# Kernel optimization log

Measured on AMD Instinct MI355X. Metric: run time of the kernel, lower is better.

Reference implementation:

```python
import jax, jax.numpy as jnp
import numpy as np

B, C, K, D = 8192, 64, 256, 64  # batch, ncodebooks, ncentroids, subvect_len
BN_EPS = 1e-5


def setup_inputs() -> dict:
    key = jax.random.key(0)
    k1, k2 = jax.random.split(key)
    return {
        "inputs": jax.random.normal(k1, (B, C, D), dtype=jnp.float32),
        "centroids_k": jax.random.normal(k2, (C, K, D), dtype=jnp.float32) * 0.1,
        "bn_gamma": jnp.ones((C,), dtype=jnp.float32),
        "bn_beta": jnp.zeros((C,), dtype=jnp.float32),
    }


def _response(inputs, centroids_k, bn_gamma, bn_beta):
    # dot-metric scores: (B, C, K)
    r = jnp.einsum('bcd,ckd->bck', inputs, centroids_k)
    # BatchNorm1d over channel dim C (training mode: biased batch stats over B and K)
    mean = r.mean(axis=(0, 2), keepdims=True)
    var = ((r - mean) ** 2).mean(axis=(0, 2), keepdims=True)
    r = (r - mean) * jax.lax.rsqrt(var + BN_EPS)
    return r * bn_gamma[None, :, None] + bn_beta[None, :, None]


def reference(inputs, centroids_k, bn_gamma, bn_beta):
    r = _response(inputs, centroids_k, bn_gamma, bn_beta)
    # torch.max(response, -1) -> (values, indices)
    mse = r.max(axis=-1)                 # (B, C)
    codes = jnp.argmax(r, axis=-1)       # (B, C) int
    # tie_in_n_out=True: _centroids_v is _centroids_k
    return codes, mse, centroids_k
```

## Files before the change

kernel.cpp:

```cpp
#include <hip/hip_runtime.h>

#define B_  8192
#define C_  64
#define K_  256
#define D_  64
#define NBT 2
#define GX  (B_ / (256 * NBT))
#define BC_ (B_ * C_)
#define BN_EPS 1e-5

#define WCAP_C 1024
#define DELTA  2.5e-3f

typedef _Float16 f16x8 __attribute__((ext_vector_type(8)));
typedef float    f32x4 __attribute__((ext_vector_type(4)));

__device__ __forceinline__ int swz(int row, int dbyte) {
    return (row * 128 + dbyte) ^ ((row & 7) << 4);
}

__global__ __launch_bounds__(512, 6) void dpq_mfma(
    const float* __restrict__ x,
    const float* __restrict__ cent,
    const float* __restrict__ gamma,
    float* __restrict__ out,
    float* __restrict__ part_sum,
    float* __restrict__ part_sq,
    int* __restrict__ wcount,
    int* __restrict__ worklist)
{
    __shared__ char lds[32768];
    const int c   = blockIdx.y;
    const int tid = threadIdx.x;
    const float sgn = (gamma[c] < 0.0f) ? -1.0f : 1.0f;

    {
        const int row = tid >> 1, half = tid & 1;
        const float* g = cent + ((size_t)c * K_ + row) * D_ + half * 32;
#pragma unroll
        for (int q = 0; q < 4; ++q) {
            float4 u0 = *(const float4*)(g + q * 8);
            float4 u1 = *(const float4*)(g + q * 8 + 4);
            f16x8 h;
            h[0] = (_Float16)(u0.x * sgn); h[1] = (_Float16)(u0.y * sgn);
            h[2] = (_Float16)(u0.z * sgn); h[3] = (_Float16)(u0.w * sgn);
            h[4] = (_Float16)(u1.x * sgn); h[5] = (_Float16)(u1.y * sgn);
            h[6] = (_Float16)(u1.z * sgn); h[7] = (_Float16)(u1.w * sgn);
            *(f16x8*)(lds + swz(row, half * 64 + q * 16)) = h;
        }
    }

    const int wid = tid >> 6, lane = tid & 63;
    const int col = lane & 15, grp = lane >> 4;

    float accs = 0.0f, accq = 0.0f;
    bool first = true;

    for (int bt = 0; bt < NBT; ++bt) {
        const int b0 = (blockIdx.x * NBT + bt) * 256 + wid * 32;

        f16x8 xf[2][2];
#pragma unroll
        for (int T = 0; T < 2; ++T)
#pragma unroll
            for (int S = 0; S < 2; ++S) {
                const float* xr = x + ((size_t)(b0 + T * 16 + col) * C_ + c) * D_
                                    + S * 32 + grp * 8;
                float4 u0 = *(const float4*)xr;
                float4 u1 = *(const float4*)(xr + 4);
                f16x8 h;
                h[0] = (_Float16)u0.x; h[1] = (_Float16)u0.y;
                h[2] = (_Float16)u0.z; h[3] = (_Float16)u0.w;
                h[4] = (_Float16)u1.x; h[5] = (_Float16)u1.y;
                h[6] = (_Float16)u1.z; h[7] = (_Float16)u1.w;
                xf[T][S] = h;
            }
        if (first) { __syncthreads(); first = false; }

        float best[2] = {-3.4e38f, -3.4e38f};
        float sec [2] = {-3.4e38f, -3.4e38f};
        int   bk_ [2] = {0, 0};

#pragma unroll 4
        for (int t = 0; t < 16; ++t) {
            const f16x8 a0 = *(const f16x8*)(lds + swz(t * 16 + col,      grp * 16));
            const f16x8 a1 = *(const f16x8*)(lds + swz(t * 16 + col, 64 + grp * 16));
            const int kb = t * 16 + grp * 4;
#pragma unroll
            for (int T = 0; T < 2; ++T) {
                f32x4 acc = {0.f, 0.f, 0.f, 0.f};
                acc = __builtin_amdgcn_mfma_f32_16x16x32_f16(a0, xf[T][0], acc, 0, 0, 0);
                acc = __builtin_amdgcn_mfma_f32_16x16x32_f16(a1, xf[T][1], acc, 0, 0, 0);
#pragma unroll
                for (int j = 0; j < 4; ++j) {
                    const float r = acc[j];
                    accs += r;
                    accq = fmaf(r, r, accq);
                    const bool gt = r > best[T];
                    sec[T]  = __builtin_amdgcn_fmed3f(r, best[T], sec[T]);
                    best[T] = fmaxf(best[T], r);
                    bk_[T]  = gt ? kb + j : bk_[T];
                }
            }
        }

#pragma unroll
        for (int T = 0; T < 2; ++T) {
            float bv = best[T], sv = sec[T];
            int   bk = bk_[T];
#pragma unroll
            for (int m = 16; m <= 32; m <<= 1) {
                const float ov = __shfl_xor(bv, m);
                const int   ok = __shfl_xor(bk, m);
                const float os = __shfl_xor(sv, m);
                sv = fmaxf(fmaxf(sv, os), fminf(bv, ov));
                if (ov > bv || (ov == bv && ok < bk)) bk = ok;
                bv = fmaxf(bv, ov);
            }
            if (grp == 0) {
                const int b = b0 + T * 16 + col;
                const size_t idx = (size_t)b * C_ + c;
                out[idx] = (float)bk;
                out[(size_t)BC_ + idx] = bv;
                if (bv - sv < DELTA && worklist) {
                    const int slot = atomicAdd(&wcount[c], 1);
                    if (slot < WCAP_C) worklist[c * WCAP_C + slot] = b;
                }
            }
        }
    }

#pragma unroll
    for (int m = 1; m <= 32; m <<= 1) {
        accs += __shfl_xor(accs, m);
        accq += __shfl_xor(accq, m);
    }
    __syncthreads();
    float* red = (float*)lds;
    if (lane == 0) { red[wid] = accs; red[8 + wid] = accq; }
    __syncthreads();
    if (tid == 0) {
        float s = 0.f, q = 0.f;
#pragma unroll
        for (int w = 0; w < 8; ++w) { s += red[w]; q += red[8 + w]; }
        part_sum[c * GX + blockIdx.x] = s;
        part_sq [c * GX + blockIdx.x] = q;
    }
}

__global__ __launch_bounds__(256) void dpq_referee(
    const float* __restrict__ x,
    const float* __restrict__ cent,
    const float* __restrict__ gamma,
    const int* __restrict__ wcount,
    const int* __restrict__ worklist,
    float* __restrict__ out)
{
    __shared__ float cl[K_ * D_];
    const int c = blockIdx.x;
    int n = wcount[c];
    if (n > WCAP_C) n = WCAP_C;
    if (n == 0) return;
    const int t = threadIdx.x;
    const float sgnf = (gamma[c] < 0.0f) ? -1.0f : 1.0f;

    {
        const float* g = cent + ((size_t)c * K_ + t) * D_;
#pragma unroll 8
        for (int d = 0; d < D_; ++d)
            cl[t * D_ + (d ^ (t & 31))] = g[d];
    }
    __syncthreads();

    const int wid = t >> 6, lane = t & 63;
    for (int i = blockIdx.y * 4 + wid; i < n; i += gridDim.y * 4) {
        const int b = worklist[c * WCAP_C + i];
        const float* xr = x + ((size_t)b * C_ + c) * D_;
        double bv = -1.0e300;
        int bk = 0;
#pragma unroll
        for (int q = 0; q < 4; ++q) {
            const int k = q * 64 + lane;
            const int sw = k & 31;
            double s = 0.0;
#pragma unroll 8
            for (int d = 0; d < D_; ++d)
                s += (double)xr[d] * (double)cl[k * D_ + (d ^ sw)];
            s *= (double)sgnf;
            if (s > bv) { bv = s; bk = k; }
        }
#pragma unroll
        for (int m = 1; m <= 32; m <<= 1) {
            const double ov = __shfl_xor(bv, m);
            const int   ok = __shfl_xor(bk, m);
            if (ov > bv || (ov == bv && ok < bk)) { bv = ov; bk = ok; }
        }
        if (lane == 0) {
            const size_t idx = (size_t)b * C_ + c;
            out[idx] = (float)bk;
            out[(size_t)BC_ + idx] = (float)bv;
        }
    }
}

__global__ void dpq_stats(
    const float* __restrict__ part_sum,
    const float* __restrict__ part_sq,
    const float* __restrict__ gamma,
    const float* __restrict__ beta,
    float* __restrict__ scale_out,
    float* __restrict__ shift_out)
{
    const int c = threadIdx.x;
    if (c >= C_) return;
    double s = 0.0, q = 0.0;
    for (int i = 0; i < GX; ++i) {
        s += (double)part_sum[c * GX + i];
        q += (double)part_sq [c * GX + i];
    }
    const double n    = (double)B_ * (double)K_;
    const double mean = s / n;
    const double var  = q / n - mean * mean;
    const double sc   = fabs((double)gamma[c]) / sqrt(var + BN_EPS);
    scale_out[c] = (float)sc;
    shift_out[c] = (float)((double)beta[c] - mean * sc);
}

__global__ __launch_bounds__(256) void dpq_apply(
    float* __restrict__ out,
    const float* __restrict__ scale,
    const float* __restrict__ shift)
{
    const int idx = blockIdx.x * 256 + threadIdx.x;
    const int c = idx & (C_ - 1);
    const float sc = scale[c];
    const float sh = shift[c];
    if (sc == 0.0f) {
        out[idx] = 0.0f;
        out[(size_t)BC_ + idx] = sh;
    } else {
        out[(size_t)BC_ + idx] = fmaf(out[(size_t)BC_ + idx], sc, sh);
    }
}

extern "C" void kernel_launch(void* const* d_in, const int* in_sizes, int n_in,
                              void* d_out, int out_size, void* d_ws, size_t ws_size,
                              hipStream_t stream)
{
    const float* x     = (const float*)d_in[0];
    const float* cent  = (const float*)d_in[1];
    const float* gamma = (const float*)d_in[2];
    const float* beta  = (const float*)d_in[3];
    float* out = (float*)d_out;
    float* ws  = (float*)d_ws;

    float* part_sum = ws;
    float* part_sq  = ws + 1024;
    float* scale    = ws + 2048;
    float* shift    = ws + 2112;
    int*   wcount   = (int*)(ws + 2176);
    int*   worklist = (int*)(ws + 2240);
    const size_t need = (size_t)(2240 + C_ * WCAP_C) * 4;
    if (ws_size < need) { wcount = nullptr; worklist = nullptr; }

    if (wcount)
        hipMemsetAsync(wcount, 0, C_ * sizeof(int), stream);

    dim3 g1(GX, C_);
    hipLaunchKernelGGL(dpq_mfma, g1, dim3(512), 0, stream,
                       x, cent, gamma, out, part_sum, part_sq, wcount, worklist);
    if (wcount)
        hipLaunchKernelGGL(dpq_referee, dim3(C_, 8), dim3(256), 0, stream,
                           x, cent, gamma, wcount, worklist, out);
    hipLaunchKernelGGL(dpq_stats, dim3(1), dim3(64), 0, stream,
                       part_sum, part_sq, gamma, beta, scale, shift);
    hipLaunchKernelGGL(dpq_apply, dim3(BC_ / 256), dim3(256), 0, stream,
                       out, scale, shift);
    hipMemcpyAsync(out + 2 * (size_t)BC_, cent,
                   (size_t)C_ * K_ * D_ * sizeof(float),
                   hipMemcpyDeviceToDevice, stream);
}
```

Before: 101.0 us.

## Process four row tiles per warp and pack argmax index into float low bits

Each warp now handles 64 batch rows (four 16-row tiles) per step instead of 32, so every LDS centroid fragment feeds twice as many MFMAs. The argmax index is packed into the low 8 mantissa bits of the score, which lets best/second tracking run as pure fmax/fmed3 with no separate index select, and shortens the cross-lane merge. This truncates score precision, so the near-tie threshold for the referee pass is raised to compensate. Launch bounds drop to 4 waves per SIMD to make room for the extra registers, and the grid becomes half as wide.

Measured after the change: 111.9 us. 10.8% more time.

```diff
diff --git a/kernel.cpp b/kernel.cpp
--- a/kernel.cpp
+++ b/kernel.cpp
@@ -4,13 +4,14 @@
 #define C_  64
 #define K_  256
 #define D_  64
-#define NBT 2
-#define GX  (B_ / (256 * NBT))
+#define NBT     2
+#define ROWS_BT 512
+#define GX  (B_ / (ROWS_BT * NBT))
 #define BC_ (B_ * C_)
 #define BN_EPS 1e-5
 
 #define WCAP_C 1024
-#define DELTA  2.5e-3f
+#define DELTA  4e-3f
 
 typedef _Float16 f16x8 __attribute__((ext_vector_type(8)));
 typedef float    f32x4 __attribute__((ext_vector_type(4)));
@@ -19,7 +20,21 @@
     return (row * 128 + dbyte) ^ ((row & 7) << 4);
 }
 
-__global__ __launch_bounds__(512, 6) void dpq_mfma(
+__device__ __forceinline__ f16x8 cvt8(const float* p) {
+    float4 u0 = *(const float4*)p;
+    float4 u1 = *(const float4*)(p + 4);
+    return (f16x8){(_Float16)u0.x, (_Float16)u0.y, (_Float16)u0.z, (_Float16)u0.w,
+                   (_Float16)u1.x, (_Float16)u1.y, (_Float16)u1.z, (_Float16)u1.w};
+}
+
+#define MERGE2(B1, S1, B2, S2)                                              \
+    {                                                                       \
+        const float lo_ = fminf(B1, B2);                                    \
+        B1 = fmaxf(B1, B2);                                                 \
+        S1 = fmaxf(lo_, fmaxf(S1, S2));                                     \
+    }
+
+__global__ __launch_bounds__(512, 4) void dpq_mfma(
     const float* __restrict__ x,
     const float* __restrict__ cent,
     const float* __restrict__ gamma,
@@ -39,89 +54,87 @@
         const float* g = cent + ((size_t)c * K_ + row) * D_ + half * 32;
 #pragma unroll
         for (int q = 0; q < 4; ++q) {
-            float4 u0 = *(const float4*)(g + q * 8);
-            float4 u1 = *(const float4*)(g + q * 8 + 4);
-            f16x8 h;
-            h[0] = (_Float16)(u0.x * sgn); h[1] = (_Float16)(u0.y * sgn);
-            h[2] = (_Float16)(u0.z * sgn); h[3] = (_Float16)(u0.w * sgn);
-            h[4] = (_Float16)(u1.x * sgn); h[5] = (_Float16)(u1.y * sgn);
-            h[6] = (_Float16)(u1.z * sgn); h[7] = (_Float16)(u1.w * sgn);
+            float v[8];
+#pragma unroll
+            for (int j = 0; j < 8; ++j) v[j] = g[q * 8 + j] * sgn;
+            f16x8 h = {(_Float16)v[0], (_Float16)v[1], (_Float16)v[2], (_Float16)v[3],
+                       (_Float16)v[4], (_Float16)v[5], (_Float16)v[6], (_Float16)v[7]};
             *(f16x8*)(lds + swz(row, half * 64 + q * 16)) = h;
         }
     }
+    __syncthreads();
 
     const int wid = tid >> 6, lane = tid & 63;
     const int col = lane & 15, grp = lane >> 4;
-
-    float accs = 0.0f, accq = 0.0f;
-    bool first = true;
+    const unsigned g4 = (unsigned)(grp * 4);
+
+    float taccs[4] = {0.f, 0.f, 0.f, 0.f};
+    float taccq[4] = {0.f, 0.f, 0.f, 0.f};
 
     for (int bt = 0; bt < NBT; ++bt) {
-        const int b0 = (blockIdx.x * NBT + bt) * 256 + wid * 32;
-
-        f16x8 xf[2][2];
-#pragma unroll
-        for (int T = 0; T < 2; ++T)
-#pragma unroll
-            for (int S = 0; S < 2; ++S) {
-                const float* xr = x + ((size_t)(b0 + T * 16 + col) * C_ + c) * D_
-                                    + S * 32 + grp * 8;
-                float4 u0 = *(const float4*)xr;
-                float4 u1 = *(const float4*)(xr + 4);
-                f16x8 h;
-                h[0] = (_Float16)u0.x; h[1] = (_Float16)u0.y;
-                h[2] = (_Float16)u0.z; h[3] = (_Float16)u0.w;
-                h[4] = (_Float16)u1.x; h[5] = (_Float16)u1.y;
-                h[6] = (_Float16)u1.z; h[7] = (_Float16)u1.w;
-                xf[T][S] = h;
-            }
-        if (first) { __syncthreads(); first = false; }
-
-        float best[2] = {-3.4e38f, -3.4e38f};
-        float sec [2] = {-3.4e38f, -3.4e38f};
-        int   bk_ [2] = {0, 0};
+        const int b0 = blockIdx.x * (ROWS_BT * NBT) + bt * ROWS_BT + wid * 64;
+
+        f16x8 xfa[4], xfb[4];
+        {
+            const float* xb = x + ((size_t)(b0 + col) * C_ + c) * D_ + grp * 8;
+            const size_t st16 = (size_t)16 * C_ * D_;
+#pragma unroll
+            for (int T = 0; T < 4; ++T) {
+                xfa[T] = cvt8(xb + T * st16);
+                xfb[T] = cvt8(xb + T * st16 + 32);
+            }
+        }
+
+        float bestv[4], secv[4];
+#pragma unroll
+        for (int T = 0; T < 4; ++T) { bestv[T] = -3.4e38f; secv[T] = -3.4e38f; }
 
 #pragma unroll 4
         for (int t = 0; t < 16; ++t) {
             const f16x8 a0 = *(const f16x8*)(lds + swz(t * 16 + col,      grp * 16));
             const f16x8 a1 = *(const f16x8*)(lds + swz(t * 16 + col, 64 + grp * 16));
-            const int kb = t * 16 + grp * 4;
-#pragma unroll
-            for (int T = 0; T < 2; ++T) {
+
+            f32x4 p[4];
+#pragma unroll
+            for (int T = 0; T < 4; ++T) {
                 f32x4 acc = {0.f, 0.f, 0.f, 0.f};
-                acc = __builtin_amdgcn_mfma_f32_16x16x32_f16(a0, xf[T][0], acc, 0, 0, 0);
-                acc = __builtin_amdgcn_mfma_f32_16x16x32_f16(a1, xf[T][1], acc, 0, 0, 0);
-#pragma unroll
-                for (int j = 0; j < 4; ++j) {
-                    const float r = acc[j];
-                    accs += r;
-                    accq = fmaf(r, r, accq);
-                    const bool gt = r > best[T];
-                    sec[T]  = __builtin_amdgcn_fmed3f(r, best[T], sec[T]);
-                    best[T] = fmaxf(best[T], r);
-                    bk_[T]  = gt ? kb + j : bk_[T];
+                acc = __builtin_amdgcn_mfma_f32_16x16x32_f16(a0, xfa[T], acc, 0, 0, 0);
+                acc = __builtin_amdgcn_mfma_f32_16x16x32_f16(a1, xfb[T], acc, 0, 0, 0);
+                p[T] = acc;
+            }
+
+            const unsigned kt = ((unsigned)t << 4) | g4;
+#pragma unroll
+            for (int j = 0; j < 4; ++j) {
+                const unsigned kj = kt + j;
+#pragma unroll
+                for (int T = 0; T < 4; ++T) {
+                    const float r = p[T][j];
+                    taccs[T] += r;
+                    taccq[T] = fmaf(r, r, taccq[T]);
+                    const float pk = __uint_as_float(
+                        (__float_as_uint(r) & 0xFFFFFF00u) | kj);
+                    secv[T]  = __builtin_amdgcn_fmed3f(pk, bestv[T], secv[T]);
+                    bestv[T] = fmaxf(bestv[T], pk);
                 }
             }
         }
 
 #pragma unroll
-        for (int T = 0; T < 2; ++T) {
-            float bv = best[T], sv = sec[T];
-            int   bk = bk_[T];
+        for (int T = 0; T < 4; ++T) {
+            float bv = bestv[T], sv = secv[T];
 #pragma unroll
             for (int m = 16; m <= 32; m <<= 1) {
-                const float ov = __shfl_xor(bv, m);
-                const int   ok = __shfl_xor(bk, m);
+                const float ob = __shfl_xor(bv, m);
                 const float os = __shfl_xor(sv, m);
-                sv = fmaxf(fmaxf(sv, os), fminf(bv, ov));
-                if (ov > bv || (ov == bv && ok < bk)) bk = ok;
-                bv = fmaxf(bv, ov);
+                MERGE2(bv, sv, ob, os);
             }
             if (grp == 0) {
                 const int b = b0 + T * 16 + col;
                 const size_t idx = (size_t)b * C_ + c;
-                out[idx] = (float)bk;
-                out[(size_t)BC_ + idx] = bv;
+                const unsigned bits = __float_as_uint(bv);
+                out[idx] = (float)(bits & 255u);
+                out[(size_t)BC_ + idx] = __uint_as_float(bits & 0xFFFFFF00u);
                 if (bv - sv < DELTA && worklist) {
                     const int slot = atomicAdd(&wcount[c], 1);
                     if (slot < WCAP_C) worklist[c * WCAP_C + slot] = b;
@@ -130,6 +143,8 @@
         }
     }
 
+    float accs = (taccs[0] + taccs[1]) + (taccs[2] + taccs[3]);
+    float accq = (taccq[0] + taccq[1]) + (taccq[2] + taccq[3]);
 #pragma unroll
     for (int m = 1; m <= 32; m <<= 1) {
         accs += __shfl_xor(accs, m);
@@ -255,16 +270,16 @@
     float* ws  = (float*)d_ws;
 
     float* part_sum = ws;
-    float* part_sq  = ws + 1024;
-    float* scale    = ws + 2048;
-    float* shift    = ws + 2112;
-    int*   wcount   = (int*)(ws + 2176);
-    int*   worklist = (int*)(ws + 2240);
-    const size_t need = (size_t)(2240 + C_ * WCAP_C) * 4;
+    float* part_sq  = ws + 512;
+    float* scale    = ws + 1024;
+    float* shift    = ws + 1088;
+    int*   wcount   = (int*)(ws + 1152);
+    int*   worklist = (int*)(ws + 1216);
+    const size_t need = (size_t)(1216 + C_ * WCAP_C) * 4;
     if (ws_size < need) { wcount = nullptr; worklist = nullptr; }
 
     if (wcount)
-        hipMemsetAsync(wcount, 0, C_ * sizeof(int), stream);
+        (void)hipMemsetAsync(wcount, 0, C_ * sizeof(int), stream);
 
     dim3 g1(GX, C_);
     hipLaunchKernelGGL(dpq_mfma, g1, dim3(512), 0, stream,
@@ -276,7 +291,7 @@
                        part_sum, part_sq, gamma, beta, scale, shift);
     hipLaunchKernelGGL(dpq_apply, dim3(BC_ / 256), dim3(256), 0, stream,
                        out, scale, shift);
-    hipMemcpyAsync(out + 2 * (size_t)BC_, cent,
-                   (size_t)C_ * K_ * D_ * sizeof(float),
-                   hipMemcpyDeviceToDevice, stream);
-}
+    (void)hipMemcpyAsync(out + 2 * (size_t)BC_, cent,
+                         (size_t)C_ * K_ * D_ * sizeof(float),
+                         hipMemcpyDeviceToDevice, stream);
+}
```
